# Kernel tuning notes

Hardware: AMD Instinct MI355X
Metric: run time of the kernel (lower is better)

Reference implementation:

```python
import jax, jax.numpy as jnp
import numpy as np

H = 8          # n_channels
NEIGHBORS = 5


def setup_inputs() -> dict:
    key = jax.random.key(0)
    k1, k2 = jax.random.split(key)
    B, N, C = 8, 1024, 256
    x = jax.random.normal(k1, (B, N, C), dtype=jnp.float32)
    # torch Linear weight: [out_features, in_features] = [2*H*C, C]
    W_qk = jax.random.normal(k2, (2 * H * C, C), dtype=jnp.float32) * (C ** -0.5)
    return {"x": x, "W_qk": W_qk}


def _forward(x, W_qk):
    B, N, C = x.shape
    scale = C ** -0.5
    qk = (x @ W_qk.T).reshape(B, N, 2, H, C).transpose(2, 0, 3, 1, 4)
    q, k = qk[0], qk[1]                              # [B,H,N,C]
    attn = jax.nn.softmax(jnp.einsum('bhnc,bhmc->bhnm', q, k) * scale, axis=-1)

    # clip(): top-k on detached channel-summed attention
    sum_edge = jnp.sum(jax.lax.stop_gradient(attn), axis=1)   # [B,N,N]
    _, index = jax.lax.top_k(sum_edge, NEIGHBORS)             # [B,N,NEIGHBORS]
    # Faithful to source: every mask row gets 1 at the union of ALL rows'
    # top-k indices (inner loop iterates over all rows of `inds`), plus eye(N).
    flat_idx = index.reshape(B, N * NEIGHBORS)                # [B, N*nb]
    col_mask = jnp.zeros((B, N), dtype=attn.dtype).at[
        jnp.arange(B)[:, None], flat_idx].set(1.0)            # [B,N]
    mask = jnp.maximum(jnp.eye(N, dtype=attn.dtype)[None], col_mask[:, None, :])  # [B,N,N]

    new_edge = mask[:, None] * attn                           # [B,H,N,N]

    # norm_edge(): row norm, then col norm, then row @ col^T
    norm_row = new_edge / (jnp.sum(new_edge, axis=-1, keepdims=True) + 1e-16)
    norm_col = norm_row / (jnp.sum(norm_row, axis=-2, keepdims=True) + 1e-16)
    return jnp.einsum('bhnm,bhkm->bhnk', norm_row, norm_col)  # [B,H,N,N]


def reference(x, W_qk):
    return _forward(x, W_qk)
```

## Files before the change

kernel.cpp:

```cpp
#include <hip/hip_runtime.h>
#include <hip/hip_bf16.h>
#include <cstdint>
#include <cstddef>

#define BB 8
#define HH 8
#define NN 1024
#define CC 256
#define YC 2048

typedef __attribute__((ext_vector_type(8))) __bf16 bf16x8;
typedef __attribute__((ext_vector_type(4))) __bf16 bf16x4;
typedef __attribute__((ext_vector_type(4))) float f32x4;

__device__ inline void async16(const void* g, void* l)
{
  __builtin_amdgcn_global_load_lds(
      reinterpret_cast<const __attribute__((address_space(1))) unsigned int*>(
          reinterpret_cast<uintptr_t>(g)),
      reinterpret_cast<__attribute__((address_space(3))) unsigned int*>(
          reinterpret_cast<uintptr_t>(l)),
      16, 0, 0);
}

__device__ inline float waveMax(float v) {
#pragma unroll
  for (int o = 32; o > 0; o >>= 1) v = fmaxf(v, __shfl_xor(v, o, 64));
  return v;
}
__device__ inline float waveSum(float v) {
#pragma unroll
  for (int o = 32; o > 0; o >>= 1) v += __shfl_xor(v, o, 64);
  return v;
}

__global__ __launch_bounds__(256) void split_kernel(const float* __restrict__ in,
                                                    __bf16* __restrict__ hi,
                                                    __bf16* __restrict__ lo)
{
  const int i = blockIdx.x * 256 + threadIdx.x;
  const float4 v = ((const float4*)in)[i];
  bf16x4 h, l;
  h.x = (__bf16)v.x; l.x = (__bf16)(v.x - (float)h.x);
  h.y = (__bf16)v.y; l.y = (__bf16)(v.y - (float)h.y);
  h.z = (__bf16)v.z; l.z = (__bf16)(v.z - (float)h.z);
  h.w = (__bf16)v.w; l.w = (__bf16)(v.w - (float)h.w);
  ((bf16x4*)hi)[i] = h;
  ((bf16x4*)lo)[i] = l;
}

__global__ __launch_bounds__(256) void wt_split_kernel(const float* __restrict__ W,
                                                       __bf16* __restrict__ Th,
                                                       __bf16* __restrict__ Tl)
{
  const int z = blockIdx.z;
  const float* Wb = W + ((size_t)z << 16);
  __shared__ float t[64][65];
  const int i0 = blockIdx.x * 64, c0 = blockIdx.y * 64;
  const int tr = threadIdx.x >> 6;
  const int tc = threadIdx.x & 63;
#pragma unroll
  for (int rr = 0; rr < 64; rr += 4)
    t[rr + tr][tc] = Wb[(size_t)(i0 + rr + tr) * 256 + c0 + tc];
  __syncthreads();
  __bf16* Thb = Th + ((size_t)z << 16);
  __bf16* Tlb = Tl + ((size_t)z << 16);
#pragma unroll
  for (int cc = 0; cc < 64; cc += 4) {
    const int c = cc + tr, i = tc;
    const float v = t[i][c];
    const __bf16 h = (__bf16)v;
    Thb[(size_t)(c0 + c) * 256 + i0 + i] = h;
    Tlb[(size_t)(c0 + c) * 256 + i0 + i] = (__bf16)(v - (float)h);
  }
}

__global__ __launch_bounds__(256) void pp_mfma_kernel(
    const __bf16* __restrict__ Th, const __bf16* __restrict__ Tl,
    __bf16* __restrict__ Phi, __bf16* __restrict__ Plo)
{
  const int h = blockIdx.z;
  const __bf16* Ah = Th + ((size_t)(8 + h) << 16);
  const __bf16* Al = Tl + ((size_t)(8 + h) << 16);
  const __bf16* Bh = Th + ((size_t)h << 16);
  const __bf16* Bl = Tl + ((size_t)h << 16);

  __shared__ __bf16 AsH[128 * 32], AsL[128 * 32], BsH[128 * 32], BsL[128 * 32];

  const int tid = threadIdx.x, lane = tid & 63, wid = tid >> 6;
  const int wr = wid >> 1, wc = wid & 1;
  const int bM = blockIdx.y * 128, bN = blockIdx.x * 128;

  const int srow = wid * 16 + (lane >> 2);
  const int scol = (lane & 3) * 8;
  const __bf16* gAh = Ah + (size_t)(bM + srow) * CC + scol;
  const __bf16* gAl = Al + (size_t)(bM + srow) * CC + scol;
  const __bf16* gBh = Bh + (size_t)(bN + srow) * CC + scol;
  const __bf16* gBl = Bl + (size_t)(bN + srow) * CC + scol;
  char* lAh = (char*)AsH + wid * 16 * 64;
  char* lAl = (char*)AsL + wid * 16 * 64;
  char* lBh = (char*)BsH + wid * 16 * 64;
  char* lBl = (char*)BsL + wid * 16 * 64;

  f32x4 acc[4][4];
  const f32x4 z4 = {0.f, 0.f, 0.f, 0.f};
#pragma unroll
  for (int m = 0; m < 4; ++m)
#pragma unroll
    for (int n = 0; n < 4; ++n) acc[m][n] = z4;

  for (int k0 = 0; k0 < CC; k0 += 32) {
    async16(gAh + k0, lAh); async16(gAh + k0 + 64 * CC, lAh + 64 * 64);
    async16(gAl + k0, lAl); async16(gAl + k0 + 64 * CC, lAl + 64 * 64);
    async16(gBh + k0, lBh); async16(gBh + k0 + 64 * CC, lBh + 64 * 64);
    async16(gBl + k0, lBl); async16(gBl + k0 + 64 * CC, lBl + 64 * 64);
    __syncthreads();

    bf16x8 ah[4], al[4], bh_[4], bl_[4];
    const int fb = (lane & 15) * 64 + (lane >> 4) * 16;
#pragma unroll
    for (int m = 0; m < 4; ++m) {
      ah[m] = *(const bf16x8*)((const char*)AsH + (wr * 64 + m * 16) * 64 + fb);
      al[m] = *(const bf16x8*)((const char*)AsL + (wr * 64 + m * 16) * 64 + fb);
    }
#pragma unroll
    for (int n = 0; n < 4; ++n) {
      bh_[n] = *(const bf16x8*)((const char*)BsH + (wc * 64 + n * 16) * 64 + fb);
      bl_[n] = *(const bf16x8*)((const char*)BsL + (wc * 64 + n * 16) * 64 + fb);
    }
#pragma unroll
    for (int m = 0; m < 4; ++m)
#pragma unroll
      for (int n = 0; n < 4; ++n) {
        acc[m][n] = __builtin_amdgcn_mfma_f32_16x16x32_bf16(al[m], bh_[n], acc[m][n], 0, 0, 0);
        acc[m][n] = __builtin_amdgcn_mfma_f32_16x16x32_bf16(ah[m], bl_[n], acc[m][n], 0, 0, 0);
        acc[m][n] = __builtin_amdgcn_mfma_f32_16x16x32_bf16(ah[m], bh_[n], acc[m][n], 0, 0, 0);
      }
    __syncthreads();
  }

  const int fr = lane & 15;
  const int fq = lane >> 4;
#pragma unroll
  for (int m = 0; m < 4; ++m) {
    const int row0 = h * 256 + bM + wr * 64 + m * 16 + fq * 4;
#pragma unroll
    for (int n = 0; n < 4; ++n) {
      const int col = bN + wc * 64 + n * 16 + fr;
#pragma unroll
      for (int r = 0; r < 4; ++r) {
        const float v = acc[m][n][r];
        const __bf16 hh = (__bf16)v;
        Phi[(size_t)(row0 + r) * CC + col] = hh;
        Plo[(size_t)(row0 + r) * CC + col] = (__bf16)(v - (float)hh);
      }
    }
  }
}

__global__ __launch_bounds__(256) void y_mfma_kernel(
    const __bf16* __restrict__ Ah, const __bf16* __restrict__ Al,
    const __bf16* __restrict__ Bh, const __bf16* __restrict__ Bl,
    __bf16* __restrict__ Chi, __bf16* __restrict__ Clo)
{
  __shared__ __bf16 AsH[128 * 32], AsL[128 * 32], BsH[128 * 32], BsL[128 * 32];

  const int tid = threadIdx.x, lane = tid & 63, wid = tid >> 6;
  const int wr = wid >> 1, wc = wid & 1;
  const int bM = blockIdx.y * 128, bN = blockIdx.x * 128;

  const int srow = wid * 16 + (lane >> 2);
  const int scol = (lane & 3) * 8;
  const __bf16* gAh = Ah + (size_t)(bM + srow) * CC + scol;
  const __bf16* gAl = Al + (size_t)(bM + srow) * CC + scol;
  const __bf16* gBh = Bh + (size_t)(bN + srow) * CC + scol;
  const __bf16* gBl = Bl + (size_t)(bN + srow) * CC + scol;
  char* lAh = (char*)AsH + wid * 16 * 64;
  char* lAl = (char*)AsL + wid * 16 * 64;
  char* lBh = (char*)BsH + wid * 16 * 64;
  char* lBl = (char*)BsL + wid * 16 * 64;

  f32x4 acc[4][4];
  const f32x4 z = {0.f, 0.f, 0.f, 0.f};
#pragma unroll
  for (int m = 0; m < 4; ++m)
#pragma unroll
    for (int n = 0; n < 4; ++n) acc[m][n] = z;

  for (int k0 = 0; k0 < CC; k0 += 32) {
    async16(gAh + k0, lAh); async16(gAh + k0 + 64 * CC, lAh + 64 * 64);
    async16(gAl + k0, lAl); async16(gAl + k0 + 64 * CC, lAl + 64 * 64);
    async16(gBh + k0, lBh); async16(gBh + k0 + 64 * CC, lBh + 64 * 64);
    async16(gBl + k0, lBl); async16(gBl + k0 + 64 * CC, lBl + 64 * 64);
    __syncthreads();

    bf16x8 ah[4], al[4], bh_[4], bl_[4];
    const int fb = (lane & 15) * 64 + (lane >> 4) * 16;
#pragma unroll
    for (int m = 0; m < 4; ++m) {
      ah[m] = *(const bf16x8*)((const char*)AsH + (wr * 64 + m * 16) * 64 + fb);
      al[m] = *(const bf16x8*)((const char*)AsL + (wr * 64 + m * 16) * 64 + fb);
    }
#pragma unroll
    for (int n = 0; n < 4; ++n) {
      bh_[n] = *(const bf16x8*)((const char*)BsH + (wc * 64 + n * 16) * 64 + fb);
      bl_[n] = *(const bf16x8*)((const char*)BsL + (wc * 64 + n * 16) * 64 + fb);
    }
#pragma unroll
    for (int m = 0; m < 4; ++m)
#pragma unroll
      for (int n = 0; n < 4; ++n) {
        acc[m][n] = __builtin_amdgcn_mfma_f32_16x16x32_bf16(al[m], bh_[n], acc[m][n], 0, 0, 0);
        acc[m][n] = __builtin_amdgcn_mfma_f32_16x16x32_bf16(ah[m], bl_[n], acc[m][n], 0, 0, 0);
        acc[m][n] = __builtin_amdgcn_mfma_f32_16x16x32_bf16(ah[m], bh_[n], acc[m][n], 0, 0, 0);
      }
    __syncthreads();
  }

  const int fr = lane & 15;
  const int fq = lane >> 4;
#pragma unroll
  for (int m = 0; m < 4; ++m) {
    const int row0 = bM + wr * 64 + m * 16 + fq * 4;
#pragma unroll
    for (int n = 0; n < 4; ++n) {
      const int col = bN + wc * 64 + n * 16 + fr;
#pragma unroll
      for (int r = 0; r < 4; ++r) {
        const float v = acc[m][n][r];
        const __bf16 h = (__bf16)v;
        Chi[(size_t)(row0 + r) * YC + col] = h;
        Clo[(size_t)(row0 + r) * YC + col] = (__bf16)(v - (float)h);
      }
    }
  }
}

__global__ __launch_bounds__(256) void qkt_mfma_kernel(
    const __bf16* __restrict__ Yh, const __bf16* __restrict__ Yl,
    const __bf16* __restrict__ Xh, const __bf16* __restrict__ Xl,
    float* __restrict__ outall)
{
  const int f = blockIdx.x;
  const int xcd = f & 7;
  const int g = f >> 3;
  const int bh = xcd + 8 * (g >> 6);
  const int tile = g & 63;
  const int b = bh >> 3, h = bh & 7;
  const size_t aoff = (size_t)b * NN * YC + (size_t)h * CC;
  const size_t boff = (size_t)b * NN * CC;
  float* C = outall + ((size_t)bh << 20);

  __shared__ __bf16 AsH[2][128 * 32], AsL[2][128 * 32];
  __shared__ __bf16 BsH[2][128 * 32], BsL[2][128 * 32];

  const int tid = threadIdx.x, lane = tid & 63, wid = tid >> 6;
  const int wr = wid >> 1, wc = wid & 1;
  const int bM = (tile >> 3) * 128, bN = (tile & 7) * 128;

  const int srow = wid * 16 + (lane >> 2);
  const int scol = (lane & 3) * 8;
  const __bf16* gAh = Yh + aoff + (size_t)(bM + srow) * YC + scol;
  const __bf16* gAl = Yl + aoff + (size_t)(bM + srow) * YC + scol;
  const __bf16* gBh = Xh + boff + (size_t)(bN + srow) * CC + scol;
  const __bf16* gBl = Xl + boff + (size_t)(bN + srow) * CC + scol;
  const int lofs = wid * 16 * 64;

  f32x4 acc[4][4];
  const f32x4 z = {0.f, 0.f, 0.f, 0.f};
#pragma unroll
  for (int m = 0; m < 4; ++m)
#pragma unroll
    for (int n = 0; n < 4; ++n) acc[m][n] = z;

  const int fb = (lane & 15) * 64 + (lane >> 4) * 16;

#define QKT_STAGE(buf, k0_)                                                    \
  do {                                                                         \
    async16(gAh + (k0_), (char*)AsH[buf] + lofs);                              \
    async16(gAh + (k0_) + (size_t)64 * YC, (char*)AsH[buf] + lofs + 64 * 64);  \
    async16(gAl + (k0_), (char*)AsL[buf] + lofs);                              \
    async16(gAl + (k0_) + (size_t)64 * YC, (char*)AsL[buf] + lofs + 64 * 64);  \
    async16(gBh + (k0_), (char*)BsH[buf] + lofs);                              \
    async16(gBh + (k0_) + (size_t)64 * CC, (char*)BsH[buf] + lofs + 64 * 64);  \
    async16(gBl + (k0_), (char*)BsL[buf] + lofs);                              \
    async16(gBl + (k0_) + (size_t)64 * CC, (char*)BsL[buf] + lofs + 64 * 64);  \
  } while (0)

#define QKT_COMPUTE(buf)                                                       \
  do {                                                                         \
    bf16x8 ah[4], al[4], bh_[4], bl_[4];                                       \
    _Pragma("unroll")                                                          \
    for (int m = 0; m < 4; ++m) {                                              \
      ah[m] = *(const bf16x8*)((const char*)AsH[buf] + (wr * 64 + m * 16) * 64 + fb); \
      al[m] = *(const bf16x8*)((const char*)AsL[buf] + (wr * 64 + m * 16) * 64 + fb); \
    }                                                                          \
    _Pragma("unroll")                                                          \
    for (int n = 0; n < 4; ++n) {                                              \
      bh_[n] = *(const bf16x8*)((const char*)BsH[buf] + (wc * 64 + n * 16) * 64 + fb); \
      bl_[n] = *(const bf16x8*)((const char*)BsL[buf] + (wc * 64 + n * 16) * 64 + fb); \
    }                                                                          \
    _Pragma("unroll")                                                          \
    for (int m = 0; m < 4; ++m)                                                \
      _Pragma("unroll")                                                        \
      for (int n = 0; n < 4; ++n) {                                            \
        acc[m][n] = __builtin_amdgcn_mfma_f32_16x16x32_bf16(al[m], bh_[n], acc[m][n], 0, 0, 0); \
        acc[m][n] = __builtin_amdgcn_mfma_f32_16x16x32_bf16(ah[m], bl_[n], acc[m][n], 0, 0, 0); \
        acc[m][n] = __builtin_amdgcn_mfma_f32_16x16x32_bf16(ah[m], bh_[n], acc[m][n], 0, 0, 0); \
      }                                                                        \
  } while (0)

  QKT_STAGE(0, 0);

  int cur = 0;
#pragma unroll 1
  for (int k0 = 0; k0 < CC - 32; k0 += 32) {
    QKT_STAGE(cur ^ 1, k0 + 32);
    asm volatile("s_waitcnt vmcnt(8)" ::: "memory");
    __builtin_amdgcn_s_barrier();
    __builtin_amdgcn_sched_barrier(0);
    QKT_COMPUTE(cur);
    __builtin_amdgcn_s_barrier();
    __builtin_amdgcn_sched_barrier(0);
    cur ^= 1;
  }
  asm volatile("s_waitcnt vmcnt(0)" ::: "memory");
  __builtin_amdgcn_s_barrier();
  __builtin_amdgcn_sched_barrier(0);
  QKT_COMPUTE(cur);

#undef QKT_STAGE
#undef QKT_COMPUTE

  const int fr = lane & 15;
  const int fq = lane >> 4;
#pragma unroll
  for (int m = 0; m < 4; ++m) {
    const int row0 = bM + wr * 64 + m * 16 + fq * 4;
#pragma unroll
    for (int n = 0; n < 4; ++n) {
      const int col = bN + wc * 64 + n * 16 + fr;
#pragma unroll
      for (int r = 0; r < 4; ++r)
        C[(size_t)(row0 + r) * NN + col] = acc[m][n][r] * 0.0625f;
    }
  }
}

__global__ __launch_bounds__(256) void softmax_se_kernel(const float* __restrict__ logits,
                                                         __bf16* __restrict__ attnb,
                                                         float* __restrict__ se)
{
  const int bn = blockIdx.x;
  const int b = bn >> 10;
  const int n = bn & 1023;
  const int t = threadIdx.x;
  const int lane = t & 63, wv = t >> 6;
  __shared__ float wred[4];
  float4 acc = make_float4(0.f, 0.f, 0.f, 0.f);

#pragma unroll 1
  for (int h = 0; h < HH; ++h) {
    const size_t rowbase = (((size_t)(b * HH + h) << 10) + n) << 10;
    const float* ar = logits + rowbase;
    __bf16* arb = attnb + rowbase;
    float4 x = *(const float4*)(ar + (t << 2));
    float mx = waveMax(fmaxf(fmaxf(x.x, x.y), fmaxf(x.z, x.w)));
    if (lane == 0) wred[wv] = mx;
    __syncthreads();
    const float M = fmaxf(fmaxf(wred[0], wred[1]), fmaxf(wred[2], wred[3]));
    __syncthreads();

    float e0 = expf(x.x - M), e1 = expf(x.y - M), e2 = expf(x.z - M), e3 = expf(x.w - M);
    float s = waveSum(e0 + e1 + e2 + e3);
    if (lane == 0) wred[wv] = s;
    __syncthreads();
    const float inv = 1.0f / (wred[0] + wred[1] + wred[2] + wred[3]);

    const float o0 = e0 * inv, o1 = e1 * inv, o2 = e2 * inv, o3 = e3 * inv;
    bf16x4 ob; ob.x = (__bf16)o0; ob.y = (__bf16)o1; ob.z = (__bf16)o2; ob.w = (__bf16)o3;
    *(bf16x4*)(arb + (t << 2)) = ob;
    acc.x += o0; acc.y += o1; acc.z += o2; acc.w += o3;
    __syncthreads();
  }
  *(float4*)(se + (size_t)bn * NN + (t << 2)) = acc;
}

__global__ __launch_bounds__(256) void topk_kernel(const float* __restrict__ se,
                                                   float* __restrict__ colmask)
{
  const int bn = blockIdx.x;
  const int b = bn >> 10;
  const int t = threadIdx.x;
  __shared__ float vals[NN];
  __shared__ unsigned long long red[256];
  const float* rowp = se + (size_t)bn * NN;
  for (int i = t; i < NN; i += 256) vals[i] = rowp[i];
  __syncthreads();

  for (int it = 0; it < 5; ++it) {
    unsigned long long best = 0ull;
    for (int i = t; i < NN; i += 256) {
      const float v = vals[i];
      if (v >= 0.f) {
        unsigned long long key =
            ((unsigned long long)__float_as_uint(v) << 32) | (unsigned)(NN - 1 - i);
        if (key > best) best = key;
      }
    }
    red[t] = best; __syncthreads();
    for (int s = 128; s > 0; s >>= 1) {
      if (t < s) red[t] = red[t] > red[t+s] ? red[t] : red[t+s];
      __syncthreads();
    }
    if (t == 0) {
      const int idx = NN - 1 - (int)(red[0] & 0xFFFFFFFFull);
      colmask[b * NN + idx] = 1.0f;
      vals[idx] = -1.0f;
    }
    __syncthreads();
  }
}

__global__ __launch_bounds__(256) void cs_rs_kernel(const __bf16* __restrict__ attnb,
                                                    const float* __restrict__ colmask,
                                                    float* __restrict__ inv_rs,
                                                    float* __restrict__ part)
{
  const int bh = blockIdx.y;
  const int b = bh >> 3;
  const int chunk = blockIdx.x;
  const int t = threadIdx.x, lane = t & 63, wv = t >> 6;
  const __bf16* ab = attnb + ((size_t)bh << 20);
  const float* cm = colmask + b * NN;
  const int c0 = lane * 16;

  float cmv[16];
#pragma unroll
  for (int q = 0; q < 4; ++q) {
    const float4 c4 = *(const float4*)(cm + c0 + q * 4);
    cmv[q*4+0] = c4.x; cmv[q*4+1] = c4.y; cmv[q*4+2] = c4.z; cmv[q*4+3] = c4.w;
  }

  float a[16];
#pragma unroll
  for (int j = 0; j < 16; ++j) a[j] = 0.f;

  const int nbase = chunk * 64 + wv * 16;
#pragma unroll 1
  for (int r = 0; r < 16; ++r) {
    const int n = nbase + r;
    const __bf16* rowp = ab + ((size_t)n << 10) + c0;
    const bf16x8 v0 = *(const bf16x8*)(rowp);
    const bf16x8 v1 = *(const bf16x8*)(rowp + 8);
    float e[16];
    float rsum = 0.f;
#pragma unroll
    for (int j = 0; j < 8; ++j) {
      const float val = ((cmv[j] != 0.f) || (c0 + j == n)) ? (float)v0[j] : 0.f;
      e[j] = val; rsum += val;
    }
#pragma unroll
    for (int j = 0; j < 8; ++j) {
      const float val = ((cmv[8+j] != 0.f) || (c0 + 8 + j == n)) ? (float)v1[j] : 0.f;
      e[8+j] = val; rsum += val;
    }
    rsum = waveSum(rsum);
    const float ir = 1.0f / (rsum + 1e-16f);
    if (lane == 0) inv_rs[bh * NN + n] = ir;
#pragma unroll
    for (int j = 0; j < 16; ++j) a[j] += e[j] * ir;
  }

  __shared__ float l[4][NN];
#pragma unroll
  for (int j = 0; j < 16; ++j) l[wv][c0 + j] = a[j];
  __syncthreads();
  const int m0 = t << 2;
  float4 o;
  o.x = l[0][m0+0] + l[1][m0+0] + l[2][m0+0] + l[3][m0+0];
  o.y = l[0][m0+1] + l[1][m0+1] + l[2][m0+1] + l[3][m0+1];
  o.z = l[0][m0+2] + l[1][m0+2] + l[2][m0+2] + l[3][m0+2];
  o.w = l[0][m0+3] + l[1][m0+3] + l[2][m0+3] + l[3][m0+3];
  *(float4*)(part + (((size_t)chunk * (BB*HH) + bh) << 10) + m0) = o;
}

__global__ __launch_bounds__(256) void cs_fin_kernel(const float* __restrict__ part,
                                                     float* __restrict__ isc)
{
  const int bh = blockIdx.x;
  const int m0 = threadIdx.x << 2;
  float a0 = 0.f, a1 = 0.f, a2 = 0.f, a3 = 0.f;
#pragma unroll
  for (int c = 0; c < 16; ++c) {
    const float4 p = *(const float4*)(part + (((size_t)c * (BB*HH) + bh) << 10) + m0);
    a0 += p.x; a1 += p.y; a2 += p.z; a3 += p.w;
  }
  float4 o;
  o.x = 1.0f / sqrtf(a0 + 1e-16f);
  o.y = 1.0f / sqrtf(a1 + 1e-16f);
  o.z = 1.0f / sqrtf(a2 + 1e-16f);
  o.w = 1.0f / sqrtf(a3 + 1e-16f);
  *(float4*)(isc + ((size_t)bh << 10) + m0) = o;
}

__global__ __launch_bounds__(256) void g_kernel(const __bf16* __restrict__ attnb,
                                                const float* __restrict__ colmask,
                                                const float* __restrict__ inv_rs,
                                                const float* __restrict__ isc,
                                                __bf16* __restrict__ Gb)
{
  const size_t idx = ((size_t)blockIdx.x * 256 + threadIdx.x) << 3;
  const size_t row = idx >> 10;
  const int m = (int)(idx & 1023);
  const int n = (int)(row & 1023);
  const int bh = (int)(row >> 10);
  const int b = bh >> 3;
  const bf16x8 vb = *(const bf16x8*)(attnb + idx);
  const float4 c0 = *(const float4*)(colmask + b * NN + m);
  const float4 c1 = *(const float4*)(colmask + b * NN + m + 4);
  const float4 s0 = *(const float4*)(isc + ((size_t)bh << 10) + m);
  const float4 s1 = *(const float4*)(isc + ((size_t)bh << 10) + m + 4);
  const float ir = inv_rs[row];
  const float cm[8] = {c0.x, c0.y, c0.z, c0.w, c1.x, c1.y, c1.z, c1.w};
  const float sc[8] = {s0.x, s0.y, s0.z, s0.w, s1.x, s1.y, s1.z, s1.w};
  bf16x8 o;
#pragma unroll
  for (int j = 0; j < 8; ++j) {
    const float e = ((cm[j] != 0.f) || (m + j == n)) ? (float)vb[j] : 0.f;
    o[j] = (__bf16)(e * ir * sc[j]);
  }
  *(bf16x8*)(Gb + idx) = o;
}

__global__ __launch_bounds__(256) void ggt_mfma_kernel(const __bf16* __restrict__ Gball,
                                                       float* __restrict__ outall)
{
  const int f = blockIdx.x;
  const int xcd = f & 7;
  const int g = f >> 3;
  const int bh = xcd + 8 * (g / 36);
  int tt = g % 36;

  const __bf16* A = Gball + ((size_t)bh << 20);
  float* C = outall + ((size_t)bh << 20);

  int ti = 0;
#pragma unroll
  for (int r = 0; r < 8; ++r) {
    const int len = 8 - r;
    if (tt < len) { ti = r; break; }
    tt -= len;
  }
  const int tj = ti + tt;

  __shared__ __bf16 As[2][128 * 32];
  __shared__ __bf16 Bs[2][128 * 32];

  const int tid  = threadIdx.x;
  const int lane = tid & 63;
  const int wid  = tid >> 6;
  const int wr   = wid >> 1;
  const int wc   = wid & 1;
  const int bM   = ti * 128;
  const int bN   = tj * 128;

  const int srow = wid * 16 + (lane >> 2);
  const int scol = (lane & 3) * 8;
  const __bf16* gA = A + (size_t)(bM + srow) * NN + scol;
  const __bf16* gB = A + (size_t)(bN + srow) * NN + scol;
  const int lofs = wid * 16 * 64;

  f32x4 acc[4][4];
  const f32x4 z = {0.f, 0.f, 0.f, 0.f};
#pragma unroll
  for (int m = 0; m < 4; ++m)
#pragma unroll
    for (int n = 0; n < 4; ++n) acc[m][n] = z;

  const int fb = (lane & 15) * 64 + (lane >> 4) * 16;

  async16(gA,           (char*)As[0] + lofs);
  async16(gA + 64 * NN, (char*)As[0] + lofs + 64 * 64);
  async16(gB,           (char*)Bs[0] + lofs);
  async16(gB + 64 * NN, (char*)Bs[0] + lofs + 64 * 64);

  int cur = 0;
#pragma unroll 1
  for (int k0 = 0; k0 < NN - 32; k0 += 32) {
    const int nxt = cur ^ 1;
    async16(gA + k0 + 32,           (char*)As[nxt] + lofs);
    async16(gA + k0 + 32 + 64 * NN, (char*)As[nxt] + lofs + 64 * 64);
    async16(gB + k0 + 32,           (char*)Bs[nxt] + lofs);
    async16(gB + k0 + 32 + 64 * NN, (char*)Bs[nxt] + lofs + 64 * 64);
    asm volatile("s_waitcnt vmcnt(4)" ::: "memory");
    __builtin_amdgcn_s_barrier();
    __builtin_amdgcn_sched_barrier(0);

    bf16x8 a[4], b[4];
#pragma unroll
    for (int m = 0; m < 4; ++m)
      a[m] = *(const bf16x8*)((const char*)As[cur] + (wr * 64 + m * 16) * 64 + fb);
#pragma unroll
    for (int n = 0; n < 4; ++n)
      b[n] = *(const bf16x8*)((const char*)Bs[cur] + (wc * 64 + n * 16) * 64 + fb);
#pragma unroll
    for (int m = 0; m < 4; ++m)
#pragma unroll
      for (int n = 0; n < 4; ++n)
        acc[m][n] = __builtin_amdgcn_mfma_f32_16x16x32_bf16(a[m], b[n], acc[m][n], 0, 0, 0);
    __builtin_amdgcn_s_barrier();
    __builtin_amdgcn_sched_barrier(0);
    cur ^= 1;
  }

  asm volatile("s_waitcnt vmcnt(0)" ::: "memory");
  __builtin_amdgcn_s_barrier();
  __builtin_amdgcn_sched_barrier(0);
  {
    bf16x8 a[4], b[4];
#pragma unroll
    for (int m = 0; m < 4; ++m)
      a[m] = *(const bf16x8*)((const char*)As[cur] + (wr * 64 + m * 16) * 64 + fb);
#pragma unroll
    for (int n = 0; n < 4; ++n)
      b[n] = *(const bf16x8*)((const char*)Bs[cur] + (wc * 64 + n * 16) * 64 + fb);
#pragma unroll
    for (int m = 0; m < 4; ++m)
#pragma unroll
      for (int n = 0; n < 4; ++n)
        acc[m][n] = __builtin_amdgcn_mfma_f32_16x16x32_bf16(a[m], b[n], acc[m][n], 0, 0, 0);
  }

  const int fr = lane & 15;
  const int fq = lane >> 4;
#pragma unroll
  for (int m = 0; m < 4; ++m) {
    const int row0 = bM + wr * 64 + m * 16 + fq * 4;
#pragma unroll
    for (int n = 0; n < 4; ++n) {
      const int col = bN + wc * 64 + n * 16 + fr;
#pragma unroll
      for (int r = 0; r < 4; ++r)
        C[(size_t)(row0 + r) * NN + col] = acc[m][n][r];
    }
  }
  if (ti != tj) {
#pragma unroll
    for (int m = 0; m < 4; ++m) {
      const int colT = bM + wr * 64 + m * 16 + fq * 4;
#pragma unroll
      for (int n = 0; n < 4; ++n) {
        const int rowT = bN + wc * 64 + n * 16 + fr;
        *(f32x4*)(C + (size_t)rowT * NN + colT) = acc[m][n];
      }
    }
  }
}

extern "C" void kernel_launch(void* const* d_in, const int* in_sizes, int n_in,
                              void* d_out, int out_size, void* d_ws, size_t ws_size,
                              hipStream_t stream)
{
  const float* x = (const float*)d_in[0];
  const float* W = (const float*)d_in[1];
  float* logits = (float*)d_out;
  char* ws = (char*)d_ws;

  __bf16* y_hi  = (__bf16*)(ws + ((size_t)0   << 20));
  __bf16* y_lo  = (__bf16*)(ws + ((size_t)32  << 20));
  __bf16* attnb = (__bf16*)(ws + ((size_t)0   << 20));
  __bf16* x_hi  = (__bf16*)(ws + ((size_t)128 << 20));
  __bf16* x_lo  = (__bf16*)(ws + ((size_t)132 << 20));
  __bf16* T_hi  = (__bf16*)(ws + ((size_t)136 << 20));
  __bf16* T_lo  = (__bf16*)(ws + ((size_t)138 << 20));
  __bf16* P_hi  = (__bf16*)(ws + ((size_t)140 << 20));
  __bf16* P_lo  = (__bf16*)(ws + ((size_t)142 << 20));
  float*  se    = (float*)(ws + ((size_t)144 << 20));
  float*  cmask = (float*)(ws + ((size_t)176 << 20));
  float*  irs   = (float*)(ws + ((size_t)177 << 20));
  float*  isc   = (float*)(ws + ((size_t)178 << 20));
  float*  csp   = (float*)(ws + ((size_t)180 << 20));
  __bf16* Gb    = (__bf16*)(ws + ((size_t)192 << 20));

  hipLaunchKernelGGL(split_kernel, dim3(BB*NN*CC/4/256), dim3(256), 0, stream,
                     x, x_hi, x_lo);
  hipLaunchKernelGGL(wt_split_kernel, dim3(4, 4, 16), dim3(256), 0, stream,
                     W, T_hi, T_lo);
  hipLaunchKernelGGL(pp_mfma_kernel, dim3(2, 2, 8), dim3(256), 0, stream,
                     T_hi, T_lo, P_hi, P_lo);

  hipLaunchKernelGGL(y_mfma_kernel, dim3(YC/128, (BB*NN)/128, 1), dim3(256), 0, stream,
                     x_hi, x_lo, P_hi, P_lo, y_hi, y_lo);

  hipLaunchKernelGGL(qkt_mfma_kernel, dim3(64 * 64), dim3(256), 0, stream,
                     y_hi, y_lo, x_hi, x_lo, logits);

  hipLaunchKernelGGL(softmax_se_kernel, dim3(BB*NN), dim3(256), 0, stream,
                     logits, attnb, se);

  hipMemsetAsync(cmask, 0, (size_t)BB * NN * 4, stream);
  hipLaunchKernelGGL(topk_kernel, dim3(BB*NN), dim3(256), 0, stream, se, cmask);

  hipLaunchKernelGGL(cs_rs_kernel, dim3(16, BB*HH), dim3(256), 0, stream,
                     attnb, cmask, irs, csp);
  hipLaunchKernelGGL(cs_fin_kernel, dim3(BB*HH), dim3(256), 0, stream, csp, isc);

  hipLaunchKernelGGL(g_kernel, dim3((BB*HH*NN*(long long)NN) / 8 / 256), dim3(256), 0, stream,
                     attnb, cmask, irs, isc, Gb);

  hipLaunchKernelGGL(ggt_mfma_kernel, dim3(36 * 64), dim3(256), 0, stream,
                     Gb, logits);

  (void)in_sizes; (void)n_in; (void)out_size; (void)ws_size;
}
```

Measured before the change: 508.3 us.

## Double-buffer y GEMM, merge split kernels, use wave-shuffle top-k reduction

Three separate changes. The y_mfma GEMM now double-buffers its LDS tiles, prefetching the next K slice with async global-to-LDS loads while computing the current one, so load latency is hidden behind MFMA work at the cost of twice the LDS footprint. The x split and W transpose-split kernels are merged into one launch to save launch overhead. The top-k argmax reduction replaces a 256-entry LDS tree, which needed a barrier at every step, with wave shuffles plus a 4-entry combine.

```diff
diff --git a/kernel.cpp b/kernel.cpp
--- a/kernel.cpp
+++ b/kernel.cpp
@@ -8,6 +8,7 @@
 #define NN 1024
 #define CC 256
 #define YC 2048
+#define NSPLIT (BB*NN*CC/4/256)
 
 typedef __attribute__((ext_vector_type(8))) __bf16 bf16x8;
 typedef __attribute__((ext_vector_type(4))) __bf16 bf16x4;
@@ -34,29 +35,29 @@
   return v;
 }
 
-__global__ __launch_bounds__(256) void split_kernel(const float* __restrict__ in,
-                                                    __bf16* __restrict__ hi,
-                                                    __bf16* __restrict__ lo)
-{
-  const int i = blockIdx.x * 256 + threadIdx.x;
-  const float4 v = ((const float4*)in)[i];
-  bf16x4 h, l;
-  h.x = (__bf16)v.x; l.x = (__bf16)(v.x - (float)h.x);
-  h.y = (__bf16)v.y; l.y = (__bf16)(v.y - (float)h.y);
-  h.z = (__bf16)v.z; l.z = (__bf16)(v.z - (float)h.z);
-  h.w = (__bf16)v.w; l.w = (__bf16)(v.w - (float)h.w);
-  ((bf16x4*)hi)[i] = h;
-  ((bf16x4*)lo)[i] = l;
-}
-
-__global__ __launch_bounds__(256) void wt_split_kernel(const float* __restrict__ W,
-                                                       __bf16* __restrict__ Th,
-                                                       __bf16* __restrict__ Tl)
-{
-  const int z = blockIdx.z;
+__global__ __launch_bounds__(256) void prep_kernel(
+    const float* __restrict__ x, const float* __restrict__ W,
+    __bf16* __restrict__ xh, __bf16* __restrict__ xl,
+    __bf16* __restrict__ Th, __bf16* __restrict__ Tl)
+{
+  __shared__ float t[64][65];
+  if (blockIdx.x < NSPLIT) {
+    const int i = blockIdx.x * 256 + threadIdx.x;
+    const float4 v = ((const float4*)x)[i];
+    bf16x4 h, l;
+    h.x = (__bf16)v.x; l.x = (__bf16)(v.x - (float)h.x);
+    h.y = (__bf16)v.y; l.y = (__bf16)(v.y - (float)h.y);
+    h.z = (__bf16)v.z; l.z = (__bf16)(v.z - (float)h.z);
+    h.w = (__bf16)v.w; l.w = (__bf16)(v.w - (float)h.w);
+    ((bf16x4*)xh)[i] = h;
+    ((bf16x4*)xl)[i] = l;
+    return;
+  }
+  const int bid = blockIdx.x - NSPLIT;
+  const int z = bid >> 4;
+  const int tile = bid & 15;
+  const int i0 = (tile & 3) * 64, c0 = (tile >> 2) * 64;
   const float* Wb = W + ((size_t)z << 16);
-  __shared__ float t[64][65];
-  const int i0 = blockIdx.x * 64, c0 = blockIdx.y * 64;
   const int tr = threadIdx.x >> 6;
   const int tc = threadIdx.x & 63;
 #pragma unroll
@@ -163,7 +164,8 @@
     const __bf16* __restrict__ Bh, const __bf16* __restrict__ Bl,
     __bf16* __restrict__ Chi, __bf16* __restrict__ Clo)
 {
-  __shared__ __bf16 AsH[128 * 32], AsL[128 * 32], BsH[128 * 32], BsL[128 * 32];
+  __shared__ __bf16 AsH[2][128 * 32], AsL[2][128 * 32];
+  __shared__ __bf16 BsH[2][128 * 32], BsL[2][128 * 32];
 
   const int tid = threadIdx.x, lane = tid & 63, wid = tid >> 6;
   const int wr = wid >> 1, wc = wid & 1;
@@ -175,10 +177,7 @@
   const __bf16* gAl = Al + (size_t)(bM + srow) * CC + scol;
   const __bf16* gBh = Bh + (size_t)(bN + srow) * CC + scol;
   const __bf16* gBl = Bl + (size_t)(bN + srow) * CC + scol;
-  char* lAh = (char*)AsH + wid * 16 * 64;
-  char* lAl = (char*)AsL + wid * 16 * 64;
-  char* lBh = (char*)BsH + wid * 16 * 64;
-  char* lBl = (char*)BsL + wid * 16 * 64;
+  const int lofs = wid * 16 * 64;
 
   f32x4 acc[4][4];
   const f32x4 z = {0.f, 0.f, 0.f, 0.f};
@@ -187,35 +186,63 @@
 #pragma unroll
     for (int n = 0; n < 4; ++n) acc[m][n] = z;
 
-  for (int k0 = 0; k0 < CC; k0 += 32) {
-    async16(gAh + k0, lAh); async16(gAh + k0 + 64 * CC, lAh + 64 * 64);
-    async16(gAl + k0, lAl); async16(gAl + k0 + 64 * CC, lAl + 64 * 64);
-    async16(gBh + k0, lBh); async16(gBh + k0 + 64 * CC, lBh + 64 * 64);
-    async16(gBl + k0, lBl); async16(gBl + k0 + 64 * CC, lBl + 64 * 64);
-    __syncthreads();
-
-    bf16x8 ah[4], al[4], bh_[4], bl_[4];
-    const int fb = (lane & 15) * 64 + (lane >> 4) * 16;
-#pragma unroll
-    for (int m = 0; m < 4; ++m) {
-      ah[m] = *(const bf16x8*)((const char*)AsH + (wr * 64 + m * 16) * 64 + fb);
-      al[m] = *(const bf16x8*)((const char*)AsL + (wr * 64 + m * 16) * 64 + fb);
-    }
-#pragma unroll
-    for (int n = 0; n < 4; ++n) {
-      bh_[n] = *(const bf16x8*)((const char*)BsH + (wc * 64 + n * 16) * 64 + fb);
-      bl_[n] = *(const bf16x8*)((const char*)BsL + (wc * 64 + n * 16) * 64 + fb);
-    }
-#pragma unroll
-    for (int m = 0; m < 4; ++m)
-#pragma unroll
-      for (int n = 0; n < 4; ++n) {
-        acc[m][n] = __builtin_amdgcn_mfma_f32_16x16x32_bf16(al[m], bh_[n], acc[m][n], 0, 0, 0);
-        acc[m][n] = __builtin_amdgcn_mfma_f32_16x16x32_bf16(ah[m], bl_[n], acc[m][n], 0, 0, 0);
-        acc[m][n] = __builtin_amdgcn_mfma_f32_16x16x32_bf16(ah[m], bh_[n], acc[m][n], 0, 0, 0);
-      }
-    __syncthreads();
-  }
+  const int fb = (lane & 15) * 64 + (lane >> 4) * 16;
+
+#define Y_STAGE(buf, k0_)                                                      \
+  do {                                                                         \
+    async16(gAh + (k0_), (char*)AsH[buf] + lofs);                              \
+    async16(gAh + (k0_) + 64 * CC, (char*)AsH[buf] + lofs + 64 * 64);          \
+    async16(gAl + (k0_), (char*)AsL[buf] + lofs);                              \
+    async16(gAl + (k0_) + 64 * CC, (char*)AsL[buf] + lofs + 64 * 64);          \
+    async16(gBh + (k0_), (char*)BsH[buf] + lofs);                              \
+    async16(gBh + (k0_) + 64 * CC, (char*)BsH[buf] + lofs + 64 * 64);          \
+    async16(gBl + (k0_), (char*)BsL[buf] + lofs);                              \
+    async16(gBl + (k0_) + 64 * CC, (char*)BsL[buf] + lofs + 64 * 64);          \
+  } while (0)
+
+#define Y_COMPUTE(buf)                                                         \
+  do {                                                                         \
+    bf16x8 ah[4], al[4], bh_[4], bl_[4];                                       \
+    _Pragma("unroll")                                                          \
+    for (int m = 0; m < 4; ++m) {                                              \
+      ah[m] = *(const bf16x8*)((const char*)AsH[buf] + (wr * 64 + m * 16) * 64 + fb); \
+      al[m] = *(const bf16x8*)((const char*)AsL[buf] + (wr * 64 + m * 16) * 64 + fb); \
+    }                                                                          \
+    _Pragma("unroll")                                                          \
+    for (int n = 0; n < 4; ++n) {                                              \
+      bh_[n] = *(const bf16x8*)((const char*)BsH[buf] + (wc * 64 + n * 16) * 64 + fb); \
+      bl_[n] = *(const bf16x8*)((const char*)BsL[buf] + (wc * 64 + n * 16) * 64 + fb); \
+    }                                                                          \
+    _Pragma("unroll")                                                          \
+    for (int m = 0; m < 4; ++m)                                                \
+      _Pragma("unroll")                                                        \
+      for (int n = 0; n < 4; ++n) {                                            \
+        acc[m][n] = __builtin_amdgcn_mfma_f32_16x16x32_bf16(al[m], bh_[n], acc[m][n], 0, 0, 0); \
+        acc[m][n] = __builtin_amdgcn_mfma_f32_16x16x32_bf16(ah[m], bl_[n], acc[m][n], 0, 0, 0); \
+        acc[m][n] = __builtin_amdgcn_mfma_f32_16x16x32_bf16(ah[m], bh_[n], acc[m][n], 0, 0, 0); \
+      }                                                                        \
+  } while (0)
+
+  Y_STAGE(0, 0);
+  int cur = 0;
+#pragma unroll 1
+  for (int k0 = 0; k0 < CC - 32; k0 += 32) {
+    Y_STAGE(cur ^ 1, k0 + 32);
+    asm volatile("s_waitcnt vmcnt(8)" ::: "memory");
+    __builtin_amdgcn_s_barrier();
+    __builtin_amdgcn_sched_barrier(0);
+    Y_COMPUTE(cur);
+    __builtin_amdgcn_s_barrier();
+    __builtin_amdgcn_sched_barrier(0);
+    cur ^= 1;
+  }
+  asm volatile("s_waitcnt vmcnt(0)" ::: "memory");
+  __builtin_amdgcn_s_barrier();
+  __builtin_amdgcn_sched_barrier(0);
+  Y_COMPUTE(cur);
+
+#undef Y_STAGE
+#undef Y_COMPUTE
 
   const int fr = lane & 15;
   const int fq = lane >> 4;
@@ -311,7 +338,6 @@
   } while (0)
 
   QKT_STAGE(0, 0);
-
   int cur = 0;
 #pragma unroll 1
   for (int k0 = 0; k0 < CC - 32; k0 += 32) {
@@ -392,8 +418,9 @@
   const int bn = blockIdx.x;
   const int b = bn >> 10;
   const int t = threadIdx.x;
+  const int lane = t & 63, wv = t >> 6;
   __shared__ float vals[NN];
-  __shared__ unsigned long long red[256];
+  __shared__ unsigned long long wbest[4];
   const float* rowp = se + (size_t)bn * NN;
   for (int i = t; i < NN; i += 256) vals[i] = rowp[i];
   __syncthreads();
@@ -408,13 +435,19 @@
         if (key > best) best = key;
       }
     }
-    red[t] = best; __syncthreads();
-    for (int s = 128; s > 0; s >>= 1) {
-      if (t < s) red[t] = red[t] > red[t+s] ? red[t] : red[t+s];
-      __syncthreads();
-    }
+#pragma unroll
+    for (int o = 32; o > 0; o >>= 1) {
+      const unsigned long long other = __shfl_xor(best, o, 64);
+      if (other > best) best = other;
+    }
+    if (lane == 0) wbest[wv] = best;
+    __syncthreads();
     if (t == 0) {
-      const int idx = NN - 1 - (int)(red[0] & 0xFFFFFFFFull);
+      unsigned long long bb = wbest[0];
+      if (wbest[1] > bb) bb = wbest[1];
+      if (wbest[2] > bb) bb = wbest[2];
+      if (wbest[3] > bb) bb = wbest[3];
+      const int idx = NN - 1 - (int)(bb & 0xFFFFFFFFull);
       colmask[b * NN + idx] = 1.0f;
       vals[idx] = -1.0f;
     }
@@ -683,10 +716,8 @@
   float*  csp   = (float*)(ws + ((size_t)180 << 20));
   __bf16* Gb    = (__bf16*)(ws + ((size_t)192 << 20));
 
-  hipLaunchKernelGGL(split_kernel, dim3(BB*NN*CC/4/256), dim3(256), 0, stream,
-                     x, x_hi, x_lo);
-  hipLaunchKernelGGL(wt_split_kernel, dim3(4, 4, 16), dim3(256), 0, stream,
-                     W, T_hi, T_lo);
+  hipLaunchKernelGGL(prep_kernel, dim3(NSPLIT + 256), dim3(256), 0, stream,
+                     x, W, x_hi, x_lo, T_hi, T_lo);
   hipLaunchKernelGGL(pp_mfma_kernel, dim3(2, 2, 8), dim3(256), 0, stream,
                      T_hi, T_lo, P_hi, P_lo);
 
```

Result: no change. 512.7 us, median of 2 (+0.9%).
